# Performance work log

Hardware: AMD Instinct MI355X
Metric: run time of the kernel (lower is better)

The kernel has to match this reference:

```python
import jax, jax.numpy as jnp
import numpy as np

H = 1024       # hidden_size
V = 32000      # output_vocab_size
STEPS = 375    # fixed greedy decode length in the original loop


def setup_inputs() -> dict:
    key = jax.random.key(0)
    ks = jax.random.split(key, 6)
    s = 0.02  # init scale
    return {
        "encoder_hidden": jax.random.normal(ks[0], (1, 1, H), dtype=jnp.float32),
        "emb": jax.random.normal(ks[1], (V, H), dtype=jnp.float32) * s,
        "W_ih": jax.random.normal(ks[2], (3 * H, H), dtype=jnp.float32) * s,   # [W_ir;W_iz;W_in]
        "W_hh": jax.random.normal(ks[3], (3 * H, H), dtype=jnp.float32) * s,   # [W_hr;W_hz;W_hn]
        "b_ih": jnp.zeros((3 * H,), dtype=jnp.float32),
        "b_hh": jnp.zeros((3 * H,), dtype=jnp.float32),
        "lin_W": jax.random.normal(ks[4], (V, H), dtype=jnp.float32) * s,
        "lin_b": jnp.zeros((V,), dtype=jnp.float32),
    }


def _gru_cell(x, h, W_ih, W_hh, b_ih, b_hh):
    # PyTorch GRU gate math (gate order r, z, n)
    gi = W_ih @ x + b_ih            # [3H]
    gh = W_hh @ h + b_hh            # [3H]
    i_r, i_z, i_n = jnp.split(gi, 3)
    h_r, h_z, h_n = jnp.split(gh, 3)
    r = jax.nn.sigmoid(i_r + h_r)
    z = jax.nn.sigmoid(i_z + h_z)
    n = jnp.tanh(i_n + r * h_n)
    return (1.0 - z) * n + z * h


def reference(encoder_hidden, emb, W_ih, W_hh, b_ih, b_hh, lin_W, lin_b):
    h0 = encoder_hidden[0, 0]  # [H], batch=1, single layer

    def step(carry, _):
        h, tok = carry
        x = emb[tok]                                   # embedding lookup [H]
        h_new = _gru_cell(x, h, W_ih, W_hh, b_ih, b_hh)
        logits = lin_W @ h_new + lin_b                 # [V]
        logp = jax.nn.log_softmax(logits)              # LogSoftmax(dim=1) on [1,V]
        next_tok = jnp.argmax(logp).astype(jnp.int32)  # greedy feedback
        return (h_new, next_tok), logp

    (h_final, _), outs = jax.lax.scan(
        step, (h0, jnp.int32(0)), None, length=STEPS)
    # original cats [1,V] outputs along dim 0 -> [STEPS, V]
    return outs, h_final.reshape(1, 1, H)
```

## Files before the change

### kernel.cpp

```cpp
#include <hip/hip_runtime.h>

#define H 1024
#define V 32000
#define STEPS 375
#define NB1 256
#define NB2 512
#define RPB1 125

__device__ __forceinline__ float dot4(const float4 a, const float4 b) {
    return fmaf(a.x, b.x, fmaf(a.y, b.y, fmaf(a.z, b.z, a.w * b.w)));
}

__device__ __forceinline__ float wave_sum(float v) {
#pragma unroll
    for (int off = 32; off > 0; off >>= 1) v += __shfl_xor(v, off);
    return v;
}

__device__ __forceinline__ void sm_merge(float& m, float& ss, int& a,
                                         float om, float os, int oa) {
    if (om > m || (om == m && oa < a)) {
        ss = os + ss * expf(m - om); m = om; a = oa;
    } else {
        ss += os * expf(om - m);
    }
}

__global__ void init_kernel(const float* __restrict__ enc, float* __restrict__ h0) {
    for (int i = threadIdx.x; i < H; i += 256) h0[i] = enc[i];
}

__global__ __launch_bounds__(256) void gru_kernel(
    const float* __restrict__ emb, const float* __restrict__ W_ih,
    const float* __restrict__ W_hh, const float* __restrict__ b_ih,
    const float* __restrict__ b_hh, const float* __restrict__ h_cur,
    float* __restrict__ h_next, float* __restrict__ out_prev,
    const float* __restrict__ pm, const float* __restrict__ ps,
    const int* __restrict__ pa, int s) {
    const int tid = threadIdx.x;
    const int lane = tid & 63;
    const int wv = tid >> 6;
    const int b = blockIdx.x;

    int tok = 0;
    if (s > 0) {
        float m = -3.4e38f, ss = 0.f;
        int a = 0x7fffffff;
#pragma unroll
        for (int k = 0; k < NB2 / 64; ++k)
            sm_merge(m, ss, a, pm[k * 64 + lane], ps[k * 64 + lane], pa[k * 64 + lane]);
#pragma unroll
        for (int off = 32; off > 0; off >>= 1) {
            float om = __shfl_xor(m, off), os = __shfl_xor(ss, off);
            int oa = __shfl_xor(a, off);
            sm_merge(m, ss, a, om, os, oa);
        }
        const float logZ = m + logf(ss);
        tok = a;
        if (tid < RPB1) out_prev[b * RPB1 + tid] -= logZ;
    }

    const int i = b * 4 + wv;
    const float4* xp = (const float4*)(emb + (size_t)tok * H);
    const float4* hp = (const float4*)h_cur;
    float4 xv[4], hv[4];
#pragma unroll
    for (int j = 0; j < 4; ++j) {
        xv[j] = xp[lane + 64 * j];
        hv[j] = hp[lane + 64 * j];
    }
    const float4* wx0 = (const float4*)(W_ih + (size_t)i * H);
    const float4* wx1 = (const float4*)(W_ih + ((size_t)i + H) * H);
    const float4* wx2 = (const float4*)(W_ih + ((size_t)i + 2 * H) * H);
    const float4* wh0 = (const float4*)(W_hh + (size_t)i * H);
    const float4* wh1 = (const float4*)(W_hh + ((size_t)i + H) * H);
    const float4* wh2 = (const float4*)(W_hh + ((size_t)i + 2 * H) * H);
    float4 WX0[4], WX1[4], WX2[4], WH0[4], WH1[4], WH2[4];
#pragma unroll
    for (int j = 0; j < 4; ++j) {
        const int idx = lane + 64 * j;
        WX0[j] = wx0[idx]; WX1[j] = wx1[idx]; WX2[j] = wx2[idx];
        WH0[j] = wh0[idx]; WH1[j] = wh1[idx]; WH2[j] = wh2[idx];
    }
    float sx0 = 0, sx1 = 0, sx2 = 0, sh0 = 0, sh1 = 0, sh2 = 0;
#pragma unroll
    for (int j = 0; j < 4; ++j) {
        sx0 += dot4(WX0[j], xv[j]); sx1 += dot4(WX1[j], xv[j]); sx2 += dot4(WX2[j], xv[j]);
        sh0 += dot4(WH0[j], hv[j]); sh1 += dot4(WH1[j], hv[j]); sh2 += dot4(WH2[j], hv[j]);
    }
    sx0 = wave_sum(sx0); sx1 = wave_sum(sx1); sx2 = wave_sum(sx2);
    sh0 = wave_sum(sh0); sh1 = wave_sum(sh1); sh2 = wave_sum(sh2);
    if (lane == 0) {
        const float rg = 1.f / (1.f + expf(-((sx0 + b_ih[i]) + (sh0 + b_hh[i]))));
        const float zg = 1.f / (1.f + expf(-((sx1 + b_ih[i + H]) + (sh1 + b_hh[i + H]))));
        const float ng = tanhf((sx2 + b_ih[i + 2 * H]) + rg * (sh2 + b_hh[i + 2 * H]));
        h_next[i] = (1.f - zg) * ng + zg * h_cur[i];
    }
}

__global__ __launch_bounds__(512, 4) void logits_kernel(
    const float* __restrict__ lin_W, const float* __restrict__ lin_b,
    const float* __restrict__ h_src, float* __restrict__ orow,
    float* __restrict__ pm, float* __restrict__ ps, int* __restrict__ pa) {
    const int tid = threadIdx.x;
    const int lane = tid & 63;
    const int wv = tid >> 6;
    const int b = blockIdx.x;
    const int row0 = (b < 256) ? 63 * b : 16128 + 62 * (b - 256);
    const int nrows = (b < 256) ? 63 : 62;

    __shared__ float red_m[8], red_s[8];
    __shared__ int red_a[8];

    const float4* h4 = (const float4*)h_src;
    float4 hr[4];
#pragma unroll
    for (int j = 0; j < 4; ++j) hr[j] = h4[lane + 64 * j];

    float m = -3.4e38f, ssum = 0.f;
    int arg = 0x7fffffff;
    for (int r = wv; r < nrows; r += 32) {
        const int rB = r + 8, rC = r + 16, rD = r + 24;
        const bool vB = rB < nrows, vC = rC < nrows, vD = rD < nrows;
        const float4* pA = (const float4*)(lin_W + (size_t)(row0 + r) * H);
        const float4* pB = (const float4*)(lin_W + (size_t)(row0 + (vB ? rB : r)) * H);
        const float4* pC = (const float4*)(lin_W + (size_t)(row0 + (vC ? rC : r)) * H);
        const float4* pD = (const float4*)(lin_W + (size_t)(row0 + (vD ? rD : r)) * H);
        float4 wA[4], wB[4], wC[4], wD[4];
#pragma unroll
        for (int j = 0; j < 4; ++j) {
            const int idx = lane + 64 * j;
            wA[j] = pA[idx]; wB[j] = pB[idx]; wC[j] = pC[idx]; wD[j] = pD[idx];
        }
        __builtin_amdgcn_sched_barrier(0);
        float aA = 0, aB = 0, aC = 0, aD = 0;
#pragma unroll
        for (int j = 0; j < 4; ++j) {
            aA += dot4(wA[j], hr[j]); aB += dot4(wB[j], hr[j]);
            aC += dot4(wC[j], hr[j]); aD += dot4(wD[j], hr[j]);
        }
        aA = wave_sum(aA); aB = wave_sum(aB);
        aC = wave_sum(aC); aD = wave_sum(aD);
        aA += lin_b[row0 + r];
        if (lane == 0) __builtin_nontemporal_store(aA, &orow[row0 + r]);
        if (aA > m) { ssum *= expf(m - aA); m = aA; arg = row0 + r; }
        ssum += expf(aA - m);
        if (vB) {
            aB += lin_b[row0 + rB];
            if (lane == 0) __builtin_nontemporal_store(aB, &orow[row0 + rB]);
            if (aB > m) { ssum *= expf(m - aB); m = aB; arg = row0 + rB; }
            ssum += expf(aB - m);
        }
        if (vC) {
            aC += lin_b[row0 + rC];
            if (lane == 0) __builtin_nontemporal_store(aC, &orow[row0 + rC]);
            if (aC > m) { ssum *= expf(m - aC); m = aC; arg = row0 + rC; }
            ssum += expf(aC - m);
        }
        if (vD) {
            aD += lin_b[row0 + rD];
            if (lane == 0) __builtin_nontemporal_store(aD, &orow[row0 + rD]);
            if (aD > m) { ssum *= expf(m - aD); m = aD; arg = row0 + rD; }
            ssum += expf(aD - m);
        }
    }
    if (lane == 0) { red_m[wv] = m; red_s[wv] = ssum; red_a[wv] = arg; }
    __syncthreads();
    if (tid == 0) {
        float M = red_m[0], S = red_s[0];
        int A = red_a[0];
#pragma unroll
        for (int w = 1; w < 8; ++w) sm_merge(M, S, A, red_m[w], red_s[w], red_a[w]);
        pm[b] = M; ps[b] = S; pa[b] = A;
    }
}

__global__ __launch_bounds__(256) void tail_kernel(
    float* __restrict__ out_last, const float* __restrict__ pm,
    const float* __restrict__ ps, const int* __restrict__ pa,
    const float* __restrict__ h_final, float* __restrict__ out_h) {
    const int tid = threadIdx.x;
    const int lane = tid & 63;
    const int b = blockIdx.x;
    float m = -3.4e38f, ss = 0.f;
    int a = 0x7fffffff;
#pragma unroll
    for (int k = 0; k < NB2 / 64; ++k)
        sm_merge(m, ss, a, pm[k * 64 + lane], ps[k * 64 + lane], pa[k * 64 + lane]);
#pragma unroll
    for (int off = 32; off > 0; off >>= 1) {
        float om = __shfl_xor(m, off), os = __shfl_xor(ss, off);
        int oa = __shfl_xor(a, off);
        sm_merge(m, ss, a, om, os, oa);
    }
    const float logZ = m + logf(ss);
    if (tid < RPB1) out_last[b * RPB1 + tid] -= logZ;
    if (b == 0)
        for (int i = tid; i < H; i += 256) out_h[i] = h_final[i];
}

extern "C" void kernel_launch(void* const* d_in, const int* in_sizes, int n_in,
                              void* d_out, int out_size, void* d_ws, size_t ws_size,
                              hipStream_t stream) {
    const float* enc = (const float*)d_in[0];
    const float* emb = (const float*)d_in[1];
    const float* W_ih = (const float*)d_in[2];
    const float* W_hh = (const float*)d_in[3];
    const float* b_ih = (const float*)d_in[4];
    const float* b_hh = (const float*)d_in[5];
    const float* lin_W = (const float*)d_in[6];
    const float* lin_b = (const float*)d_in[7];
    float* out = (float*)d_out;
    float* ws = (float*)d_ws;

    float* h_buf = ws;
    float* pm = ws + 2 * H;
    float* ps = pm + NB2;
    int* pa = (int*)(ps + NB2);

    init_kernel<<<1, 256, 0, stream>>>(enc, h_buf);
    for (int s = 0; s < STEPS; ++s) {
        float* h_cur = h_buf + (s & 1) * H;
        float* h_next = h_buf + ((s + 1) & 1) * H;
        float* out_prev = out + (size_t)(s > 0 ? s - 1 : 0) * V;
        gru_kernel<<<NB1, 256, 0, stream>>>(emb, W_ih, W_hh, b_ih, b_hh,
                                            h_cur, h_next, out_prev,
                                            pm, ps, pa, s);
        logits_kernel<<<NB2, 512, 0, stream>>>(lin_W, lin_b, h_next,
                                               out + (size_t)s * V, pm, ps, pa);
    }
    tail_kernel<<<NB1, 256, 0, stream>>>(out + (size_t)(STEPS - 1) * V, pm, ps, pa,
                                         h_buf + (STEPS & 1) * H,
                                         out + (size_t)V * STEPS);
}
```

Before: 12.66 ms.

## Defer log-softmax normalization to a final pass and use nontemporal lin_W loads

The read-modify-write that subtracted logZ from the previous row inside every GRU step is removed. Each step now only records logZ, and one final kernel normalizes all rows in a single bulk pass. This takes scattered global read-modify-writes off the serial per-step critical path, at the cost of re-reading and rewriting the whole output once at the end. Two of the eight waves in the logits kernel also switch to nontemporal loads for lin_W, to reduce cache pollution so W_ih/W_hh can stay cached.

Measured after the change: 13.02 ms. 1.03x slower.

```diff
diff --git a/kernel.cpp b/kernel.cpp
--- a/kernel.cpp
+++ b/kernel.cpp
@@ -5,7 +5,8 @@
 #define STEPS 375
 #define NB1 256
 #define NB2 512
-#define RPB1 125
+
+typedef float vfloat4 __attribute__((ext_vector_type(4)));
 
 __device__ __forceinline__ float dot4(const float4 a, const float4 b) {
     return fmaf(a.x, b.x, fmaf(a.y, b.y, fmaf(a.z, b.z, a.w * b.w)));
@@ -26,6 +27,20 @@
     }
 }
 
+__device__ __forceinline__ void load_row4(const float4* p, int lane, float4 w[4], bool nt) {
+    if (nt) {
+        const vfloat4* q = (const vfloat4*)p;
+#pragma unroll
+        for (int j = 0; j < 4; ++j) {
+            vfloat4 t = __builtin_nontemporal_load(&q[lane + 64 * j]);
+            w[j] = make_float4(t.x, t.y, t.z, t.w);
+        }
+    } else {
+#pragma unroll
+        for (int j = 0; j < 4; ++j) w[j] = p[lane + 64 * j];
+    }
+}
+
 __global__ void init_kernel(const float* __restrict__ enc, float* __restrict__ h0) {
     for (int i = threadIdx.x; i < H; i += 256) h0[i] = enc[i];
 }
@@ -34,7 +49,7 @@
     const float* __restrict__ emb, const float* __restrict__ W_ih,
     const float* __restrict__ W_hh, const float* __restrict__ b_ih,
     const float* __restrict__ b_hh, const float* __restrict__ h_cur,
-    float* __restrict__ h_next, float* __restrict__ out_prev,
+    float* __restrict__ h_next, float* __restrict__ logz,
     const float* __restrict__ pm, const float* __restrict__ ps,
     const int* __restrict__ pa, int s) {
     const int tid = threadIdx.x;
@@ -55,9 +70,8 @@
             int oa = __shfl_xor(a, off);
             sm_merge(m, ss, a, om, os, oa);
         }
-        const float logZ = m + logf(ss);
         tok = a;
-        if (tid < RPB1) out_prev[b * RPB1 + tid] -= logZ;
+        if (b == 0 && tid == 0) logz[s - 1] = m + logf(ss);
     }
 
     const int i = b * 4 + wv;
@@ -69,19 +83,13 @@
         xv[j] = xp[lane + 64 * j];
         hv[j] = hp[lane + 64 * j];
     }
-    const float4* wx0 = (const float4*)(W_ih + (size_t)i * H);
-    const float4* wx1 = (const float4*)(W_ih + ((size_t)i + H) * H);
-    const float4* wx2 = (const float4*)(W_ih + ((size_t)i + 2 * H) * H);
-    const float4* wh0 = (const float4*)(W_hh + (size_t)i * H);
-    const float4* wh1 = (const float4*)(W_hh + ((size_t)i + H) * H);
-    const float4* wh2 = (const float4*)(W_hh + ((size_t)i + 2 * H) * H);
     float4 WX0[4], WX1[4], WX2[4], WH0[4], WH1[4], WH2[4];
-#pragma unroll
-    for (int j = 0; j < 4; ++j) {
-        const int idx = lane + 64 * j;
-        WX0[j] = wx0[idx]; WX1[j] = wx1[idx]; WX2[j] = wx2[idx];
-        WH0[j] = wh0[idx]; WH1[j] = wh1[idx]; WH2[j] = wh2[idx];
-    }
+    load_row4((const float4*)(W_ih + (size_t)i * H), lane, WX0, false);
+    load_row4((const float4*)(W_ih + ((size_t)i + H) * H), lane, WX1, false);
+    load_row4((const float4*)(W_ih + ((size_t)i + 2 * H) * H), lane, WX2, false);
+    load_row4((const float4*)(W_hh + (size_t)i * H), lane, WH0, false);
+    load_row4((const float4*)(W_hh + ((size_t)i + H) * H), lane, WH1, false);
+    load_row4((const float4*)(W_hh + ((size_t)i + 2 * H) * H), lane, WH2, false);
     float sx0 = 0, sx1 = 0, sx2 = 0, sh0 = 0, sh1 = 0, sh2 = 0;
 #pragma unroll
     for (int j = 0; j < 4; ++j) {
@@ -108,6 +116,7 @@
     const int b = blockIdx.x;
     const int row0 = (b < 256) ? 63 * b : 16128 + 62 * (b - 256);
     const int nrows = (b < 256) ? 63 : 62;
+    const bool nt = (wv == 3) || (wv == 7);
 
     __shared__ float red_m[8], red_s[8];
     __shared__ int red_a[8];
@@ -122,16 +131,11 @@
     for (int r = wv; r < nrows; r += 32) {
         const int rB = r + 8, rC = r + 16, rD = r + 24;
         const bool vB = rB < nrows, vC = rC < nrows, vD = rD < nrows;
-        const float4* pA = (const float4*)(lin_W + (size_t)(row0 + r) * H);
-        const float4* pB = (const float4*)(lin_W + (size_t)(row0 + (vB ? rB : r)) * H);
-        const float4* pC = (const float4*)(lin_W + (size_t)(row0 + (vC ? rC : r)) * H);
-        const float4* pD = (const float4*)(lin_W + (size_t)(row0 + (vD ? rD : r)) * H);
         float4 wA[4], wB[4], wC[4], wD[4];
-#pragma unroll
-        for (int j = 0; j < 4; ++j) {
-            const int idx = lane + 64 * j;
-            wA[j] = pA[idx]; wB[j] = pB[idx]; wC[j] = pC[idx]; wD[j] = pD[idx];
-        }
+        load_row4((const float4*)(lin_W + (size_t)(row0 + r) * H), lane, wA, nt);
+        load_row4((const float4*)(lin_W + (size_t)(row0 + (vB ? rB : r)) * H), lane, wB, nt);
+        load_row4((const float4*)(lin_W + (size_t)(row0 + (vC ? rC : r)) * H), lane, wC, nt);
+        load_row4((const float4*)(lin_W + (size_t)(row0 + (vD ? rD : r)) * H), lane, wD, nt);
         __builtin_amdgcn_sched_barrier(0);
         float aA = 0, aB = 0, aC = 0, aD = 0;
 #pragma unroll
@@ -175,6 +179,19 @@
     }
 }
 
+__global__ __launch_bounds__(256) void final_kernel(float* __restrict__ out,
+                                                    const float* __restrict__ logz) {
+    const int row = blockIdx.x >> 3;
+    const int seg = blockIdx.x & 7;
+    const float lz = logz[row];
+    float4* p = (float4*)(out + (size_t)row * V) + seg * 1000;
+    for (int i = threadIdx.x; i < 1000; i += 256) {
+        float4 v = p[i];
+        v.x -= lz; v.y -= lz; v.z -= lz; v.w -= lz;
+        p[i] = v;
+    }
+}
+
 __global__ __launch_bounds__(256) void tail_kernel(
     float* __restrict__ out_last, const float* __restrict__ pm,
     const float* __restrict__ ps, const int* __restrict__ pa,
@@ -194,7 +211,7 @@
         sm_merge(m, ss, a, om, os, oa);
     }
     const float logZ = m + logf(ss);
-    if (tid < RPB1) out_last[b * RPB1 + tid] -= logZ;
+    if (tid < 125) out_last[b * 125 + tid] -= logZ;
     if (b == 0)
         for (int i = tid; i < H; i += 256) out_h[i] = h_final[i];
 }
@@ -217,18 +234,18 @@
     float* pm = ws + 2 * H;
     float* ps = pm + NB2;
     int* pa = (int*)(ps + NB2);
+    float* logz = (float*)(pa + NB2);
 
     init_kernel<<<1, 256, 0, stream>>>(enc, h_buf);
     for (int s = 0; s < STEPS; ++s) {
         float* h_cur = h_buf + (s & 1) * H;
         float* h_next = h_buf + ((s + 1) & 1) * H;
-        float* out_prev = out + (size_t)(s > 0 ? s - 1 : 0) * V;
         gru_kernel<<<NB1, 256, 0, stream>>>(emb, W_ih, W_hh, b_ih, b_hh,
-                                            h_cur, h_next, out_prev,
-                                            pm, ps, pa, s);
+                                            h_cur, h_next, logz, pm, ps, pa, s);
         logits_kernel<<<NB2, 512, 0, stream>>>(lin_W, lin_b, h_next,
                                                out + (size_t)s * V, pm, ps, pa);
     }
+    final_kernel<<<(STEPS - 1) * 8, 256, 0, stream>>>(out, logz);
     tail_kernel<<<NB1, 256, 0, stream>>>(out + (size_t)(STEPS - 1) * V, pm, ps, pa,
                                          h_buf + (STEPS & 1) * H,
                                          out + (size_t)V * STEPS);
```

## Compute logits from fp16 copy of lin_W with fp32 rescoring of near-max rows

Applied to the files above, without the earlier changes.

Converts lin_W to fp16 once into workspace and computes all logits per step with fdot2 on half the bytes. Rows whose fp16 logit is within a margin of the block max are recomputed in fp32 to choose the argmax exactly. The output log-probs are now fp16-accuracy, and the margin heuristic could miss the true argmax if the fp16 error exceeds DELTA. Blocks are also resized (1024 blocks of 256 threads), with an fp32 fallback kernel when the workspace is too small.

Measured after the change: 16.71 ms. 32.0% more time.

```diff
diff --git a/kernel.cpp b/kernel.cpp
--- a/kernel.cpp
+++ b/kernel.cpp
@@ -1,11 +1,15 @@
 #include <hip/hip_runtime.h>
+#include <hip/hip_fp16.h>
 
 #define H 1024
 #define V 32000
 #define STEPS 375
 #define NB1 256
-#define NB2 512
+#define NB2 1024
 #define RPB1 125
+#define DELTA 0.02f
+
+typedef _Float16 half2v __attribute__((ext_vector_type(2)));
 
 __device__ __forceinline__ float dot4(const float4 a, const float4 b) {
     return fmaf(a.x, b.x, fmaf(a.y, b.y, fmaf(a.z, b.z, a.w * b.w)));
@@ -26,8 +30,34 @@
     }
 }
 
+__device__ __forceinline__ float fdot2u(unsigned u, half2v h, float c) {
+#if __has_builtin(__builtin_amdgcn_fdot2)
+    return __builtin_amdgcn_fdot2(__builtin_bit_cast(half2v, u), h, c, false);
+#else
+    half2v w = __builtin_bit_cast(half2v, u);
+    return fmaf((float)w.y, (float)h.y, fmaf((float)w.x, (float)h.x, c));
+#endif
+}
+
 __global__ void init_kernel(const float* __restrict__ enc, float* __restrict__ h0) {
     for (int i = threadIdx.x; i < H; i += 256) h0[i] = enc[i];
+}
+
+__global__ __launch_bounds__(512) void conv_kernel(const float* __restrict__ src,
+                                                   unsigned short* __restrict__ dst) {
+    const size_t idx = (size_t)blockIdx.x * 512 + threadIdx.x;
+    const float4* s4 = (const float4*)src;
+    float4 a = s4[2 * idx], b = s4[2 * idx + 1];
+    uint4 o;
+    o.x = (unsigned)__half_as_ushort(__float2half(a.x)) |
+          ((unsigned)__half_as_ushort(__float2half(a.y)) << 16);
+    o.y = (unsigned)__half_as_ushort(__float2half(a.z)) |
+          ((unsigned)__half_as_ushort(__float2half(a.w)) << 16);
+    o.z = (unsigned)__half_as_ushort(__float2half(b.x)) |
+          ((unsigned)__half_as_ushort(__float2half(b.y)) << 16);
+    o.w = (unsigned)__half_as_ushort(__float2half(b.z)) |
+          ((unsigned)__half_as_ushort(__float2half(b.w)) << 16);
+    ((uint4*)dst)[idx] = o;
 }
 
 __global__ __launch_bounds__(256) void gru_kernel(
@@ -98,7 +128,120 @@
     }
 }
 
-__global__ __launch_bounds__(512, 4) void logits_kernel(
+__global__ __launch_bounds__(256, 4) void logits_f16_kernel(
+    const unsigned short* __restrict__ wh16, const float* __restrict__ lin_W,
+    const float* __restrict__ lin_b, const float* __restrict__ h_src,
+    float* __restrict__ orow, float* __restrict__ pm, float* __restrict__ ps,
+    int* __restrict__ pa) {
+    const int tid = threadIdx.x;
+    const int lane = tid & 63;
+    const int wv = tid >> 6;
+    const int b = blockIdx.x;
+    const int row0 = (b < 256) ? 32 * b : 8192 + 31 * (b - 256);
+    const int nrows = (b < 256) ? 32 : 31;
+
+    __shared__ float red_m[4], red_s[4];
+    __shared__ float s_cm[4];
+    __shared__ int s_ca[4];
+
+    const float4* h4 = (const float4*)h_src;
+    const float4 fa0 = h4[2 * lane], fa1 = h4[2 * lane + 1];
+    const float4 fb0 = h4[128 + 2 * lane], fb1 = h4[129 + 2 * lane];
+    half2v ha[4], hb[4];
+    ha[0] = half2v{(_Float16)fa0.x, (_Float16)fa0.y};
+    ha[1] = half2v{(_Float16)fa0.z, (_Float16)fa0.w};
+    ha[2] = half2v{(_Float16)fa1.x, (_Float16)fa1.y};
+    ha[3] = half2v{(_Float16)fa1.z, (_Float16)fa1.w};
+    hb[0] = half2v{(_Float16)fb0.x, (_Float16)fb0.y};
+    hb[1] = half2v{(_Float16)fb0.z, (_Float16)fb0.w};
+    hb[2] = half2v{(_Float16)fb1.x, (_Float16)fb1.y};
+    hb[3] = half2v{(_Float16)fb1.z, (_Float16)fb1.w};
+
+    uint4 qa[8], qb[8];
+    bool val[8];
+#pragma unroll
+    for (int k = 0; k < 8; ++k) {
+        const int rr = wv + 4 * k;
+        val[k] = rr < nrows;
+        const uint4* wp = (const uint4*)(wh16 + (size_t)(row0 + (val[k] ? rr : 0)) * H);
+        qa[k] = wp[lane];
+        qb[k] = wp[64 + lane];
+    }
+    __builtin_amdgcn_sched_barrier(0);
+
+    float lg[8];
+    float m = -3.4e38f, ssum = 0.f;
+#pragma unroll
+    for (int k = 0; k < 8; ++k) {
+        float a = 0.f;
+        a = fdot2u(qa[k].x, ha[0], a);
+        a = fdot2u(qa[k].y, ha[1], a);
+        a = fdot2u(qa[k].z, ha[2], a);
+        a = fdot2u(qa[k].w, ha[3], a);
+        a = fdot2u(qb[k].x, hb[0], a);
+        a = fdot2u(qb[k].y, hb[1], a);
+        a = fdot2u(qb[k].z, hb[2], a);
+        a = fdot2u(qb[k].w, hb[3], a);
+        a = wave_sum(a);
+        if (val[k]) {
+            const int col = row0 + wv + 4 * k;
+            a += lin_b[col];
+            lg[k] = a;
+            if (lane == 0) __builtin_nontemporal_store(a, &orow[col]);
+            if (a > m) { ssum *= expf(m - a); m = a; }
+            ssum += expf(a - m);
+        } else {
+            lg[k] = -3.4e38f;
+        }
+    }
+    if (lane == 0) { red_m[wv] = m; red_s[wv] = ssum; }
+    __syncthreads();
+
+    float Mb = fmaxf(fmaxf(red_m[0], red_m[1]), fmaxf(red_m[2], red_m[3]));
+
+    float cm = -3.4e38f;
+    int ca = 0x7fffffff;
+    float4 hv[4];
+    bool loaded = false;
+#pragma unroll
+    for (int k = 0; k < 8; ++k) {
+        if (lg[k] > Mb - DELTA) {
+            const int row = row0 + wv + 4 * k;
+            if (!loaded) {
+#pragma unroll
+                for (int j = 0; j < 4; ++j) hv[j] = h4[lane + 64 * j];
+                loaded = true;
+            }
+            const float4* rp = (const float4*)(lin_W + (size_t)row * H);
+            float a = 0.f;
+#pragma unroll
+            for (int j = 0; j < 4; ++j) a += dot4(rp[lane + 64 * j], hv[j]);
+            a = wave_sum(a) + lin_b[row];
+            if (a > cm || (a == cm && row < ca)) { cm = a; ca = row; }
+        }
+    }
+    if (lane == 0) { s_cm[wv] = cm; s_ca[wv] = ca; }
+    __syncthreads();
+    if (tid == 0) {
+        float M = red_m[0], S = red_s[0];
+#pragma unroll
+        for (int w = 1; w < 4; ++w) {
+            const float mw = red_m[w], sw = red_s[w];
+            if (mw > M) { S = sw + S * expf(M - mw); M = mw; }
+            else S += sw * expf(mw - M);
+        }
+        float CM = s_cm[0];
+        int CA = s_ca[0];
+#pragma unroll
+        for (int w = 1; w < 4; ++w)
+            if (s_cm[w] > CM || (s_cm[w] == CM && s_ca[w] < CA)) { CM = s_cm[w]; CA = s_ca[w]; }
+        pm[b] = CM;
+        ps[b] = S * expf(M - CM);
+        pa[b] = CA;
+    }
+}
+
+__global__ __launch_bounds__(256, 4) void logits_fp32_kernel(
     const float* __restrict__ lin_W, const float* __restrict__ lin_b,
     const float* __restrict__ h_src, float* __restrict__ orow,
     float* __restrict__ pm, float* __restrict__ ps, int* __restrict__ pa) {
@@ -106,11 +249,11 @@
     const int lane = tid & 63;
     const int wv = tid >> 6;
     const int b = blockIdx.x;
-    const int row0 = (b < 256) ? 63 * b : 16128 + 62 * (b - 256);
-    const int nrows = (b < 256) ? 63 : 62;
-
-    __shared__ float red_m[8], red_s[8];
-    __shared__ int red_a[8];
+    const int row0 = (b < 256) ? 32 * b : 8192 + 31 * (b - 256);
+    const int nrows = (b < 256) ? 32 : 31;
+
+    __shared__ float red_m[4], red_s[4];
+    __shared__ int red_a[4];
 
     const float4* h4 = (const float4*)h_src;
     float4 hr[4];
@@ -119,49 +262,33 @@
 
     float m = -3.4e38f, ssum = 0.f;
     int arg = 0x7fffffff;
-    for (int r = wv; r < nrows; r += 32) {
-        const int rB = r + 8, rC = r + 16, rD = r + 24;
-        const bool vB = rB < nrows, vC = rC < nrows, vD = rD < nrows;
-        const float4* pA = (const float4*)(lin_W + (size_t)(row0 + r) * H);
-        const float4* pB = (const float4*)(lin_W + (size_t)(row0 + (vB ? rB : r)) * H);
-        const float4* pC = (const float4*)(lin_W + (size_t)(row0 + (vC ? rC : r)) * H);
-        const float4* pD = (const float4*)(lin_W + (size_t)(row0 + (vD ? rD : r)) * H);
-        float4 wA[4], wB[4], wC[4], wD[4];
-#pragma unroll
-        for (int j = 0; j < 4; ++j) {
-            const int idx = lane + 64 * j;
-            wA[j] = pA[idx]; wB[j] = pB[idx]; wC[j] = pC[idx]; wD[j] = pD[idx];
+#pragma unroll
+    for (int half = 0; half < 2; ++half) {
+        float4 w[4][4];
+        int rr[4];
+        bool val[4];
+#pragma unroll
+        for (int q = 0; q < 4; ++q) {
+            rr[q] = wv + 4 * (half * 4 + q);
+            val[q] = rr[q] < nrows;
+            const float4* p = (const float4*)(lin_W + (size_t)(row0 + (val[q] ? rr[q] : 0)) * H);
+#pragma unroll
+            for (int j = 0; j < 4; ++j) w[q][j] = p[lane + 64 * j];
         }
         __builtin_amdgcn_sched_barrier(0);
-        float aA = 0, aB = 0, aC = 0, aD = 0;
-#pragma unroll
-        for (int j = 0; j < 4; ++j) {
-            aA += dot4(wA[j], hr[j]); aB += dot4(wB[j], hr[j]);
-            aC += dot4(wC[j], hr[j]); aD += dot4(wD[j], hr[j]);
-        }
-        aA = wave_sum(aA); aB = wave_sum(aB);
-        aC = wave_sum(aC); aD = wave_sum(aD);
-        aA += lin_b[row0 + r];
-        if (lane == 0) __builtin_nontemporal_store(aA, &orow[row0 + r]);
-        if (aA > m) { ssum *= expf(m - aA); m = aA; arg = row0 + r; }
-        ssum += expf(aA - m);
-        if (vB) {
-            aB += lin_b[row0 + rB];
-            if (lane == 0) __builtin_nontemporal_store(aB, &orow[row0 + rB]);
-            if (aB > m) { ssum *= expf(m - aB); m = aB; arg = row0 + rB; }
-            ssum += expf(aB - m);
-        }
-        if (vC) {
-            aC += lin_b[row0 + rC];
-            if (lane == 0) __builtin_nontemporal_store(aC, &orow[row0 + rC]);
-            if (aC > m) { ssum *= expf(m - aC); m = aC; arg = row0 + rC; }
-            ssum += expf(aC - m);
-        }
-        if (vD) {
-            aD += lin_b[row0 + rD];
-            if (lane == 0) __builtin_nontemporal_store(aD, &orow[row0 + rD]);
-            if (aD > m) { ssum *= expf(m - aD); m = aD; arg = row0 + rD; }
-            ssum += expf(aD - m);
+#pragma unroll
+        for (int q = 0; q < 4; ++q) {
+            float a = 0.f;
+#pragma unroll
+            for (int j = 0; j < 4; ++j) a += dot4(w[q][j], hr[j]);
+            a = wave_sum(a);
+            if (val[q]) {
+                const int col = row0 + rr[q];
+                a += lin_b[col];
+                if (lane == 0) __builtin_nontemporal_store(a, &orow[col]);
+                if (a > m) { ssum *= expf(m - a); m = a; arg = col; }
+                ssum += expf(a - m);
+            }
         }
     }
     if (lane == 0) { red_m[wv] = m; red_s[wv] = ssum; red_a[wv] = arg; }
@@ -170,7 +297,7 @@
         float M = red_m[0], S = red_s[0];
         int A = red_a[0];
 #pragma unroll
-        for (int w = 1; w < 8; ++w) sm_merge(M, S, A, red_m[w], red_s[w], red_a[w]);
+        for (int w = 1; w < 4; ++w) sm_merge(M, S, A, red_m[w], red_s[w], red_a[w]);
         pm[b] = M; ps[b] = S; pa[b] = A;
     }
 }
@@ -217,8 +344,13 @@
     float* pm = ws + 2 * H;
     float* ps = pm + NB2;
     int* pa = (int*)(ps + NB2);
+    unsigned short* wh16 = (unsigned short*)((char*)d_ws + 32768);
+    const size_t need = 32768 + (size_t)V * H * 2;
+    const bool f16path = ws_size >= need;
 
     init_kernel<<<1, 256, 0, stream>>>(enc, h_buf);
+    if (f16path)
+        conv_kernel<<<V * H / 8 / 512, 512, 0, stream>>>(lin_W, wh16);
     for (int s = 0; s < STEPS; ++s) {
         float* h_cur = h_buf + (s & 1) * H;
         float* h_next = h_buf + ((s + 1) & 1) * H;
@@ -226,8 +358,12 @@
         gru_kernel<<<NB1, 256, 0, stream>>>(emb, W_ih, W_hh, b_ih, b_hh,
                                             h_cur, h_next, out_prev,
                                             pm, ps, pa, s);
-        logits_kernel<<<NB2, 512, 0, stream>>>(lin_W, lin_b, h_next,
-                                               out + (size_t)s * V, pm, ps, pa);
+        if (f16path)
+            logits_f16_kernel<<<NB2, 256, 0, stream>>>(wh16, lin_W, lin_b, h_next,
+                                                       out + (size_t)s * V, pm, ps, pa);
+        else
+            logits_fp32_kernel<<<NB2, 256, 0, stream>>>(lin_W, lin_b, h_next,
+                                                        out + (size_t)s * V, pm, ps, pa);
     }
     tail_kernel<<<NB1, 256, 0, stream>>>(out + (size_t)(STEPS - 1) * V, pm, ps, pa,
                                          h_buf + (STEPS & 1) * H,
```

## Finalize softmax reduction in last logits block; hoist GRU weight loads before token

Applied to the files above, without the earlier changes.

The logits kernel now uses an atomic counter so the last-finishing block merges all per-block max/sum/argmax partials and writes the token and logZ once. Every GRU block therefore no longer redundantly reduces 512 partials, and the tail kernel shrinks. The GRU kernel issues its weight and hidden-state loads before reading the token, so the dependent embedding load overlaps with them. The logits kernel loads all 8 rows per wave up front with launch bounds relaxed to 2 waves per SIMD, trading occupancy for more loads in flight and adding one atomic plus a serialized final reduction per step.

Result: slower. 17.50 ms (+38.3%).

```diff
diff --git a/kernel.cpp b/kernel.cpp
--- a/kernel.cpp
+++ b/kernel.cpp
@@ -26,8 +26,23 @@
     }
 }
 
-__global__ void init_kernel(const float* __restrict__ enc, float* __restrict__ h0) {
+__device__ __forceinline__ void st_agent_f(float* p, float v) {
+    __hip_atomic_store(p, v, __ATOMIC_RELAXED, __HIP_MEMORY_SCOPE_AGENT);
+}
+__device__ __forceinline__ void st_agent_i(int* p, int v) {
+    __hip_atomic_store(p, v, __ATOMIC_RELAXED, __HIP_MEMORY_SCOPE_AGENT);
+}
+__device__ __forceinline__ float ld_agent_f(const float* p) {
+    return __hip_atomic_load(p, __ATOMIC_RELAXED, __HIP_MEMORY_SCOPE_AGENT);
+}
+__device__ __forceinline__ int ld_agent_i(const int* p) {
+    return __hip_atomic_load(p, __ATOMIC_RELAXED, __HIP_MEMORY_SCOPE_AGENT);
+}
+
+__global__ void init_kernel(const float* __restrict__ enc, float* __restrict__ h0,
+                            int* __restrict__ cnt) {
     for (int i = threadIdx.x; i < H; i += 256) h0[i] = enc[i];
+    for (int i = threadIdx.x; i < STEPS; i += 256) cnt[i] = 0;
 }
 
 __global__ __launch_bounds__(256) void gru_kernel(
@@ -35,53 +50,40 @@
     const float* __restrict__ W_hh, const float* __restrict__ b_ih,
     const float* __restrict__ b_hh, const float* __restrict__ h_cur,
     float* __restrict__ h_next, float* __restrict__ out_prev,
-    const float* __restrict__ pm, const float* __restrict__ ps,
-    const int* __restrict__ pa, int s) {
+    const int* __restrict__ tok_p, const float* __restrict__ logz_p, int s) {
     const int tid = threadIdx.x;
     const int lane = tid & 63;
     const int wv = tid >> 6;
     const int b = blockIdx.x;
+    const int i = b * 4 + wv;
+
+    const float4* hp = (const float4*)h_cur;
+    float4 hv[4];
+    float4 WX0[4], WX1[4], WX2[4], WH0[4], WH1[4], WH2[4];
+#pragma unroll
+    for (int j = 0; j < 4; ++j) {
+        const int idx = lane + 64 * j;
+        hv[j] = hp[idx];
+        WX0[j] = ((const float4*)(W_ih + (size_t)i * H))[idx];
+        WX1[j] = ((const float4*)(W_ih + ((size_t)i + H) * H))[idx];
+        WX2[j] = ((const float4*)(W_ih + ((size_t)i + 2 * H) * H))[idx];
+        WH0[j] = ((const float4*)(W_hh + (size_t)i * H))[idx];
+        WH1[j] = ((const float4*)(W_hh + ((size_t)i + H) * H))[idx];
+        WH2[j] = ((const float4*)(W_hh + ((size_t)i + 2 * H) * H))[idx];
+    }
 
     int tok = 0;
     if (s > 0) {
-        float m = -3.4e38f, ss = 0.f;
-        int a = 0x7fffffff;
-#pragma unroll
-        for (int k = 0; k < NB2 / 64; ++k)
-            sm_merge(m, ss, a, pm[k * 64 + lane], ps[k * 64 + lane], pa[k * 64 + lane]);
-#pragma unroll
-        for (int off = 32; off > 0; off >>= 1) {
-            float om = __shfl_xor(m, off), os = __shfl_xor(ss, off);
-            int oa = __shfl_xor(a, off);
-            sm_merge(m, ss, a, om, os, oa);
-        }
-        const float logZ = m + logf(ss);
-        tok = a;
-        if (tid < RPB1) out_prev[b * RPB1 + tid] -= logZ;
-    }
-
-    const int i = b * 4 + wv;
+        tok = tok_p[0];
+        const float lz = logz_p[0];
+        if (tid < RPB1) out_prev[b * RPB1 + tid] -= lz;
+    }
+
     const float4* xp = (const float4*)(emb + (size_t)tok * H);
-    const float4* hp = (const float4*)h_cur;
-    float4 xv[4], hv[4];
-#pragma unroll
-    for (int j = 0; j < 4; ++j) {
-        xv[j] = xp[lane + 64 * j];
-        hv[j] = hp[lane + 64 * j];
-    }
-    const float4* wx0 = (const float4*)(W_ih + (size_t)i * H);
-    const float4* wx1 = (const float4*)(W_ih + ((size_t)i + H) * H);
-    const float4* wx2 = (const float4*)(W_ih + ((size_t)i + 2 * H) * H);
-    const float4* wh0 = (const float4*)(W_hh + (size_t)i * H);
-    const float4* wh1 = (const float4*)(W_hh + ((size_t)i + H) * H);
-    const float4* wh2 = (const float4*)(W_hh + ((size_t)i + 2 * H) * H);
-    float4 WX0[4], WX1[4], WX2[4], WH0[4], WH1[4], WH2[4];
-#pragma unroll
-    for (int j = 0; j < 4; ++j) {
-        const int idx = lane + 64 * j;
-        WX0[j] = wx0[idx]; WX1[j] = wx1[idx]; WX2[j] = wx2[idx];
-        WH0[j] = wh0[idx]; WH1[j] = wh1[idx]; WH2[j] = wh2[idx];
-    }
+    float4 xv[4];
+#pragma unroll
+    for (int j = 0; j < 4; ++j) xv[j] = xp[lane + 64 * j];
+
     float sx0 = 0, sx1 = 0, sx2 = 0, sh0 = 0, sh1 = 0, sh2 = 0;
 #pragma unroll
     for (int j = 0; j < 4; ++j) {
@@ -98,10 +100,12 @@
     }
 }
 
-__global__ __launch_bounds__(512, 4) void logits_kernel(
+__global__ __launch_bounds__(512, 2) void logits_kernel(
     const float* __restrict__ lin_W, const float* __restrict__ lin_b,
     const float* __restrict__ h_src, float* __restrict__ orow,
-    float* __restrict__ pm, float* __restrict__ ps, int* __restrict__ pa) {
+    float* __restrict__ pm, float* __restrict__ ps, int* __restrict__ pa,
+    int* __restrict__ tok_out, float* __restrict__ logz_out,
+    int* __restrict__ cnt) {
     const int tid = threadIdx.x;
     const int lane = tid & 63;
     const int wv = tid >> 6;
@@ -111,57 +115,39 @@
 
     __shared__ float red_m[8], red_s[8];
     __shared__ int red_a[8];
+    __shared__ int s_last;
 
     const float4* h4 = (const float4*)h_src;
     float4 hr[4];
 #pragma unroll
     for (int j = 0; j < 4; ++j) hr[j] = h4[lane + 64 * j];
 
+    float4 w[8][4];
+    bool val[8];
+#pragma unroll
+    for (int k = 0; k < 8; ++k) {
+        const int rr = wv + 8 * k;
+        val[k] = rr < nrows;
+        const float4* p = (const float4*)(lin_W + (size_t)(row0 + (val[k] ? rr : 0)) * H);
+#pragma unroll
+        for (int j = 0; j < 4; ++j) w[k][j] = p[lane + 64 * j];
+    }
+    __builtin_amdgcn_sched_barrier(0);
+
     float m = -3.4e38f, ssum = 0.f;
     int arg = 0x7fffffff;
-    for (int r = wv; r < nrows; r += 32) {
-        const int rB = r + 8, rC = r + 16, rD = r + 24;
-        const bool vB = rB < nrows, vC = rC < nrows, vD = rD < nrows;
-        const float4* pA = (const float4*)(lin_W + (size_t)(row0 + r) * H);
-        const float4* pB = (const float4*)(lin_W + (size_t)(row0 + (vB ? rB : r)) * H);
-        const float4* pC = (const float4*)(lin_W + (size_t)(row0 + (vC ? rC : r)) * H);
-        const float4* pD = (const float4*)(lin_W + (size_t)(row0 + (vD ? rD : r)) * H);
-        float4 wA[4], wB[4], wC[4], wD[4];
-#pragma unroll
-        for (int j = 0; j < 4; ++j) {
-            const int idx = lane + 64 * j;
-            wA[j] = pA[idx]; wB[j] = pB[idx]; wC[j] = pC[idx]; wD[j] = pD[idx];
-        }
-        __builtin_amdgcn_sched_barrier(0);
-        float aA = 0, aB = 0, aC = 0, aD = 0;
-#pragma unroll
-        for (int j = 0; j < 4; ++j) {
-            aA += dot4(wA[j], hr[j]); aB += dot4(wB[j], hr[j]);
-            aC += dot4(wC[j], hr[j]); aD += dot4(wD[j], hr[j]);
-        }
-        aA = wave_sum(aA); aB = wave_sum(aB);
-        aC = wave_sum(aC); aD = wave_sum(aD);
-        aA += lin_b[row0 + r];
-        if (lane == 0) __builtin_nontemporal_store(aA, &orow[row0 + r]);
-        if (aA > m) { ssum *= expf(m - aA); m = aA; arg = row0 + r; }
-        ssum += expf(aA - m);
-        if (vB) {
-            aB += lin_b[row0 + rB];
-            if (lane == 0) __builtin_nontemporal_store(aB, &orow[row0 + rB]);
-            if (aB > m) { ssum *= expf(m - aB); m = aB; arg = row0 + rB; }
-            ssum += expf(aB - m);
-        }
-        if (vC) {
-            aC += lin_b[row0 + rC];
-            if (lane == 0) __builtin_nontemporal_store(aC, &orow[row0 + rC]);
-            if (aC > m) { ssum *= expf(m - aC); m = aC; arg = row0 + rC; }
-            ssum += expf(aC - m);
-        }
-        if (vD) {
-            aD += lin_b[row0 + rD];
-            if (lane == 0) __builtin_nontemporal_store(aD, &orow[row0 + rD]);
-            if (aD > m) { ssum *= expf(m - aD); m = aD; arg = row0 + rD; }
-            ssum += expf(aD - m);
+#pragma unroll
+    for (int k = 0; k < 8; ++k) {
+        float a = 0.f;
+#pragma unroll
+        for (int j = 0; j < 4; ++j) a += dot4(w[k][j], hr[j]);
+        a = wave_sum(a);
+        if (val[k]) {
+            const int col = row0 + wv + 8 * k;
+            a += lin_b[col];
+            if (lane == 0) __builtin_nontemporal_store(a, &orow[col]);
+            if (a > m) { ssum *= expf(m - a); m = a; arg = col; }
+            ssum += expf(a - m);
         }
     }
     if (lane == 0) { red_m[wv] = m; red_s[wv] = ssum; red_a[wv] = arg; }
@@ -170,30 +156,47 @@
         float M = red_m[0], S = red_s[0];
         int A = red_a[0];
 #pragma unroll
-        for (int w = 1; w < 8; ++w) sm_merge(M, S, A, red_m[w], red_s[w], red_a[w]);
-        pm[b] = M; ps[b] = S; pa[b] = A;
+        for (int wq = 1; wq < 8; ++wq) sm_merge(M, S, A, red_m[wq], red_s[wq], red_a[wq]);
+        st_agent_f(&pm[b], M);
+        st_agent_f(&ps[b], S);
+        st_agent_i(&pa[b], A);
+        __builtin_amdgcn_fence(__ATOMIC_RELEASE, "agent");
+        const int old = __hip_atomic_fetch_add(cnt, 1, __ATOMIC_ACQ_REL,
+                                               __HIP_MEMORY_SCOPE_AGENT);
+        s_last = (old == NB2 - 1);
+    }
+    __syncthreads();
+
+    if (s_last) {
+        __builtin_amdgcn_fence(__ATOMIC_ACQUIRE, "agent");
+        float gm = ld_agent_f(&pm[tid]);
+        float gs = ld_agent_f(&ps[tid]);
+        int ga = ld_agent_i(&pa[tid]);
+#pragma unroll
+        for (int off = 32; off > 0; off >>= 1) {
+            float om = __shfl_xor(gm, off), os = __shfl_xor(gs, off);
+            int oa = __shfl_xor(ga, off);
+            sm_merge(gm, gs, ga, om, os, oa);
+        }
+        if (lane == 0) { red_m[wv] = gm; red_s[wv] = gs; red_a[wv] = ga; }
+        __syncthreads();
+        if (tid == 0) {
+            float M = red_m[0], S = red_s[0];
+            int A = red_a[0];
+#pragma unroll
+            for (int wq = 1; wq < 8; ++wq) sm_merge(M, S, A, red_m[wq], red_s[wq], red_a[wq]);
+            tok_out[0] = A;
+            logz_out[0] = M + logf(S);
+        }
     }
 }
 
 __global__ __launch_bounds__(256) void tail_kernel(
-    float* __restrict__ out_last, const float* __restrict__ pm,
-    const float* __restrict__ ps, const int* __restrict__ pa,
+    float* __restrict__ out_last, const float* __restrict__ logz_p,
     const float* __restrict__ h_final, float* __restrict__ out_h) {
     const int tid = threadIdx.x;
-    const int lane = tid & 63;
     const int b = blockIdx.x;
-    float m = -3.4e38f, ss = 0.f;
-    int a = 0x7fffffff;
-#pragma unroll
-    for (int k = 0; k < NB2 / 64; ++k)
-        sm_merge(m, ss, a, pm[k * 64 + lane], ps[k * 64 + lane], pa[k * 64 + lane]);
-#pragma unroll
-    for (int off = 32; off > 0; off >>= 1) {
-        float om = __shfl_xor(m, off), os = __shfl_xor(ss, off);
-        int oa = __shfl_xor(a, off);
-        sm_merge(m, ss, a, om, os, oa);
-    }
-    const float logZ = m + logf(ss);
+    const float logZ = logz_p[0];
     if (tid < RPB1) out_last[b * RPB1 + tid] -= logZ;
     if (b == 0)
         for (int i = tid; i < H; i += 256) out_h[i] = h_final[i];
@@ -217,19 +220,25 @@
     float* pm = ws + 2 * H;
     float* ps = pm + NB2;
     int* pa = (int*)(ps + NB2);
-
-    init_kernel<<<1, 256, 0, stream>>>(enc, h_buf);
+    int* tok = pa + NB2;
+    float* logz = (float*)(tok + STEPS);
+    int* cnt = (int*)(logz + STEPS);
+
+    init_kernel<<<1, 256, 0, stream>>>(enc, h_buf, cnt);
     for (int s = 0; s < STEPS; ++s) {
         float* h_cur = h_buf + (s & 1) * H;
         float* h_next = h_buf + ((s + 1) & 1) * H;
         float* out_prev = out + (size_t)(s > 0 ? s - 1 : 0) * V;
+        const int sp = (s > 0) ? s - 1 : 0;
         gru_kernel<<<NB1, 256, 0, stream>>>(emb, W_ih, W_hh, b_ih, b_hh,
                                             h_cur, h_next, out_prev,
-                                            pm, ps, pa, s);
+                                            tok + sp, logz + sp, s);
         logits_kernel<<<NB2, 512, 0, stream>>>(lin_W, lin_b, h_next,
-                                               out + (size_t)s * V, pm, ps, pa);
-    }
-    tail_kernel<<<NB1, 256, 0, stream>>>(out + (size_t)(STEPS - 1) * V, pm, ps, pa,
+                                               out + (size_t)s * V, pm, ps, pa,
+                                               tok + s, logz + s, cnt + s);
+    }
+    tail_kernel<<<NB1, 256, 0, stream>>>(out + (size_t)(STEPS - 1) * V,
+                                         logz + (STEPS - 1),
                                          h_buf + (STEPS & 1) * H,
                                          out + (size_t)V * STEPS);
 }
```
